# Optimization experiments

Measured on AMD Instinct MI355X. Metric: run time of the kernel, lower is better.

## Reference

```python
import jax, jax.numpy as jnp
import numpy as np

EPS = 1e-12  # matches torch F.normalize default eps

def setup_inputs() -> dict:
    key = jax.random.key(0)
    k1, k2 = jax.random.split(key)
    N, D = 16384, 1024
    pc_feat = jax.random.normal(k1, (N, D), dtype=jnp.float32)
    aug_feat = jax.random.normal(k2, (N, D), dtype=jnp.float32)
    return {"pc_feat": pc_feat, "aug_feat": aug_feat}

def reference(pc_feat, aug_feat):
    # F.normalize(x, dim=1): x / max(||x||_2, eps)
    pc_n = pc_feat / jnp.maximum(jnp.linalg.norm(pc_feat, axis=1, keepdims=True), EPS)
    aug_n = aug_feat / jnp.maximum(jnp.linalg.norm(aug_feat, axis=1, keepdims=True), EPS)
    # diag(pc_n @ aug_n.T) == row-wise dot product; avoids the O(N^2) matmul
    cos = jnp.sum(pc_n * aug_n, axis=1)  # [N]
    # loss = sum(1 - cos) / N == mean(1 - cos)
    return jnp.mean(1.0 - cos)
```

## Files before the change

### kernel.cpp

```cpp
#include <hip/hip_runtime.h>


#define N_ROWS 16384
#define DIM_V4 256
#define TPB 256
#define WAVES_PER_BLOCK (TPB / 64)
#define BLOCKS (N_ROWS / WAVES_PER_BLOCK)

__global__ __launch_bounds__(TPB) void cos_rows_kernel(
    const float4* __restrict__ a, const float4* __restrict__ b,
    float* __restrict__ partial)
{
    const int wave = threadIdx.x >> 6;
    const int lane = threadIdx.x & 63;
    const int r = blockIdx.x * WAVES_PER_BLOCK + wave;

    const float4* ap = a + (size_t)r * DIM_V4;
    const float4* bp = b + (size_t)r * DIM_V4;

    float4 x[4], y[4];
    #pragma unroll
    for (int k = 0; k < 4; ++k) x[k] = ap[lane + 64 * k];
    #pragma unroll
    for (int k = 0; k < 4; ++k) y[k] = bp[lane + 64 * k];

    float ab = 0.0f, aa = 0.0f, bb = 0.0f;
    #pragma unroll
    for (int k = 0; k < 4; ++k) {
        ab += x[k].x * y[k].x + x[k].y * y[k].y + x[k].z * y[k].z + x[k].w * y[k].w;
        aa += x[k].x * x[k].x + x[k].y * x[k].y + x[k].z * x[k].z + x[k].w * x[k].w;
        bb += y[k].x * y[k].x + y[k].y * y[k].y + y[k].z * y[k].z + y[k].w * y[k].w;
    }

    #pragma unroll
    for (int off = 32; off > 0; off >>= 1) {
        ab += __shfl_down(ab, off);
        aa += __shfl_down(aa, off);
        bb += __shfl_down(bb, off);
    }

    __shared__ float s[WAVES_PER_BLOCK];
    if (lane == 0) {
        float na = fmaxf(sqrtf(aa), 1e-12f);
        float nb = fmaxf(sqrtf(bb), 1e-12f);
        s[wave] = ab / (na * nb);
    }
    __syncthreads();
    if (threadIdx.x == 0) {
        float t = 0.0f;
        #pragma unroll
        for (int i = 0; i < WAVES_PER_BLOCK; ++i) t += s[i];
        partial[blockIdx.x] = t;
    }
}

__global__ __launch_bounds__(1024) void finalize_kernel(
    const float* __restrict__ partial, float* __restrict__ out)
{
    const int wave = threadIdx.x >> 6;
    const int lane = threadIdx.x & 63;
    float t = 0.0f;
    #pragma unroll
    for (int i = 0; i < BLOCKS / 1024; ++i) t += partial[threadIdx.x + 1024 * i];
    #pragma unroll
    for (int off = 32; off > 0; off >>= 1) t += __shfl_down(t, off);
    __shared__ float s[1024 / 64];
    if (lane == 0) s[wave] = t;
    __syncthreads();
    if (threadIdx.x == 0) {
        float tot = 0.0f;
        #pragma unroll
        for (int i = 0; i < 1024 / 64; ++i) tot += s[i];
        out[0] = 1.0f - tot / (float)N_ROWS;
    }
}

extern "C" void kernel_launch(void* const* d_in, const int* in_sizes, int n_in,
                              void* d_out, int out_size, void* d_ws, size_t ws_size,
                              hipStream_t stream) {
    const float4* pc  = (const float4*)d_in[0];
    const float4* aug = (const float4*)d_in[1];
    float* partial = (float*)d_ws;
    float* out = (float*)d_out;

    cos_rows_kernel<<<BLOCKS, TPB, 0, stream>>>(pc, aug, partial);
    finalize_kernel<<<1, 1024, 0, stream>>>(partial, out);
}
```

Before: 141.1 us.

## Double-buffer rows through LDS with async global-to-LDS loads, multiple rows per wave

```diff
diff --git a/kernel.cpp b/kernel.cpp
--- a/kernel.cpp
+++ b/kernel.cpp
@@ -2,75 +2,118 @@
 
 
 #define N_ROWS 16384
-#define DIM_V4 256
 #define TPB 256
-#define WAVES_PER_BLOCK (TPB / 64)
-#define BLOCKS (N_ROWS / WAVES_PER_BLOCK)
+#define WPB 4
+#define RPW 8
+#define BLOCKS (N_ROWS / (WPB * RPW))
+
+typedef const __attribute__((address_space(1))) unsigned int* gas_u32;
+typedef __attribute__((address_space(3))) unsigned int* las_u32;
+
+template<int N> __device__ __forceinline__ void wait_vmcnt() {
+    asm volatile("s_waitcnt vmcnt(%0)" :: "n"(N) : "memory");
+}
+
+__device__ __forceinline__ void stage_row(const float* gA, const float* gB,
+                                          float* ldsbuf, int lane) {
+    #pragma unroll
+    for (int j = 0; j < 4; ++j)
+        __builtin_amdgcn_global_load_lds((gas_u32)(gA + j * 256 + lane * 4),
+                                         (las_u32)(ldsbuf + j * 256), 16, 0, 0);
+    #pragma unroll
+    for (int j = 0; j < 4; ++j)
+        __builtin_amdgcn_global_load_lds((gas_u32)(gB + j * 256 + lane * 4),
+                                         (las_u32)(ldsbuf + 1024 + j * 256), 16, 0, 0);
+}
+
+__device__ __forceinline__ void consume_row(const float* ldsbuf, int lane,
+                                            float& ab, float& aa, float& bb) {
+    const float4* A = (const float4*)ldsbuf;
+    const float4* B = (const float4*)(ldsbuf + 1024);
+    float4 x[4], y[4];
+    #pragma unroll
+    for (int k = 0; k < 4; ++k) { x[k] = A[lane + 64 * k]; y[k] = B[lane + 64 * k]; }
+    float tab = 0, taa = 0, tbb = 0;
+    #pragma unroll
+    for (int k = 0; k < 4; ++k) {
+        tab += x[k].x * y[k].x + x[k].y * y[k].y + x[k].z * y[k].z + x[k].w * y[k].w;
+        taa += x[k].x * x[k].x + x[k].y * x[k].y + x[k].z * x[k].z + x[k].w * x[k].w;
+        tbb += y[k].x * y[k].x + y[k].y * y[k].y + y[k].z * y[k].z + y[k].w * y[k].w;
+    }
+    ab = tab; aa = taa; bb = tbb;
+}
 
 __global__ __launch_bounds__(TPB) void cos_rows_kernel(
-    const float4* __restrict__ a, const float4* __restrict__ b,
+    const float* __restrict__ a, const float* __restrict__ b,
     float* __restrict__ partial)
 {
+    __shared__ float lds[WPB][2][2048];
+    __shared__ float s[WPB];
     const int wave = threadIdx.x >> 6;
     const int lane = threadIdx.x & 63;
-    const int r = blockIdx.x * WAVES_PER_BLOCK + wave;
+    const int r0 = (blockIdx.x * WPB + wave) * RPW;
 
-    const float4* ap = a + (size_t)r * DIM_V4;
-    const float4* bp = b + (size_t)r * DIM_V4;
+    const float* ga = a + (size_t)r0 * 1024;
+    const float* gb = b + (size_t)r0 * 1024;
 
-    float4 x[4], y[4];
+    float ab[RPW], aa[RPW], bb[RPW];
+
+    stage_row(ga, gb, lds[wave][0], lane);
     #pragma unroll
-    for (int k = 0; k < 4; ++k) x[k] = ap[lane + 64 * k];
-    #pragma unroll
-    for (int k = 0; k < 4; ++k) y[k] = bp[lane + 64 * k];
-
-    float ab = 0.0f, aa = 0.0f, bb = 0.0f;
-    #pragma unroll
-    for (int k = 0; k < 4; ++k) {
-        ab += x[k].x * y[k].x + x[k].y * y[k].y + x[k].z * y[k].z + x[k].w * y[k].w;
-        aa += x[k].x * x[k].x + x[k].y * x[k].y + x[k].z * x[k].z + x[k].w * x[k].w;
-        bb += y[k].x * y[k].x + y[k].y * y[k].y + y[k].z * y[k].z + y[k].w * y[k].w;
+    for (int i = 0; i < RPW; ++i) {
+        if (i < RPW - 1) {
+            stage_row(ga + (size_t)(i + 1) * 1024, gb + (size_t)(i + 1) * 1024,
+                      lds[wave][(i + 1) & 1], lane);
+            wait_vmcnt<8>();
+        } else {
+            wait_vmcnt<0>();
+        }
+        consume_row(lds[wave][i & 1], lane, ab[i], aa[i], bb[i]);
     }
 
     #pragma unroll
-    for (int off = 32; off > 0; off >>= 1) {
-        ab += __shfl_down(ab, off);
-        aa += __shfl_down(aa, off);
-        bb += __shfl_down(bb, off);
+    for (int i = 0; i < RPW; ++i) {
+        #pragma unroll
+        for (int off = 32; off > 0; off >>= 1) {
+            ab[i] += __shfl_down(ab[i], off);
+            aa[i] += __shfl_down(aa[i], off);
+            bb[i] += __shfl_down(bb[i], off);
+        }
     }
-
-    __shared__ float s[WAVES_PER_BLOCK];
     if (lane == 0) {
-        float na = fmaxf(sqrtf(aa), 1e-12f);
-        float nb = fmaxf(sqrtf(bb), 1e-12f);
-        s[wave] = ab / (na * nb);
+        float t = 0.0f;
+        #pragma unroll
+        for (int i = 0; i < RPW; ++i) {
+            float na = fmaxf(sqrtf(aa[i]), 1e-12f);
+            float nb = fmaxf(sqrtf(bb[i]), 1e-12f);
+            t += ab[i] / (na * nb);
+        }
+        s[wave] = t;
     }
     __syncthreads();
     if (threadIdx.x == 0) {
         float t = 0.0f;
         #pragma unroll
-        for (int i = 0; i < WAVES_PER_BLOCK; ++i) t += s[i];
+        for (int i = 0; i < WPB; ++i) t += s[i];
         partial[blockIdx.x] = t;
     }
 }
 
-__global__ __launch_bounds__(1024) void finalize_kernel(
+__global__ __launch_bounds__(512) void finalize_kernel(
     const float* __restrict__ partial, float* __restrict__ out)
 {
     const int wave = threadIdx.x >> 6;
     const int lane = threadIdx.x & 63;
-    float t = 0.0f;
-    #pragma unroll
-    for (int i = 0; i < BLOCKS / 1024; ++i) t += partial[threadIdx.x + 1024 * i];
+    float t = partial[threadIdx.x];
     #pragma unroll
     for (int off = 32; off > 0; off >>= 1) t += __shfl_down(t, off);
-    __shared__ float s[1024 / 64];
+    __shared__ float s[512 / 64];
     if (lane == 0) s[wave] = t;
     __syncthreads();
     if (threadIdx.x == 0) {
         float tot = 0.0f;
         #pragma unroll
-        for (int i = 0; i < 1024 / 64; ++i) tot += s[i];
+        for (int i = 0; i < 512 / 64; ++i) tot += s[i];
         out[0] = 1.0f - tot / (float)N_ROWS;
     }
 }
@@ -78,11 +121,11 @@
 extern "C" void kernel_launch(void* const* d_in, const int* in_sizes, int n_in,
                               void* d_out, int out_size, void* d_ws, size_t ws_size,
                               hipStream_t stream) {
-    const float4* pc  = (const float4*)d_in[0];
-    const float4* aug = (const float4*)d_in[1];
+    const float* pc  = (const float*)d_in[0];
+    const float* aug = (const float*)d_in[1];
     float* partial = (float*)d_ws;
     float* out = (float*)d_out;
 
     cos_rows_kernel<<<BLOCKS, TPB, 0, stream>>>(pc, aug, partial);
-    finalize_kernel<<<1, 1024, 0, stream>>>(partial, out);
+    finalize_kernel<<<1, 512, 0, stream>>>(partial, out);
 }
```

New measurement: 146.5 us. 3.8% more time.
